# Kernel tuning notes

Measured on AMD Instinct MI355X. Metric: run time of the kernel, lower is better.

The kernel has to match this reference:

```python
import jax, jax.numpy as jnp
import numpy as np

N_NODES = 50000
N_EDGES = 25000
NNZ = 800000
IN_DIM = 256
OUT_DIM = 256


def setup_inputs() -> dict:
    key = jax.random.key(0)
    k1, k2, k3, k4, k5 = jax.random.split(key, 5)
    X = jax.random.normal(k1, (N_NODES, IN_DIM), dtype=jnp.float32)
    node_idx = jax.random.randint(k2, (NNZ,), 0, N_NODES, dtype=jnp.int64)
    edge_idx = jax.random.randint(k3, (NNZ,), 0, N_EDGES, dtype=jnp.int64)
    # Xavier-uniform-ish weight, zero bias (matches reset_parameters)
    limit = float(np.sqrt(6.0 / (IN_DIM + OUT_DIM)))
    W = jax.random.uniform(k4, (IN_DIM, OUT_DIM), dtype=jnp.float32, minval=-limit, maxval=limit)
    b = jnp.zeros((OUT_DIM,), dtype=jnp.float32)
    return {"X": X, "node_idx": node_idx, "edge_idx": edge_idx, "W": W, "b": b}


def reference(X, node_idx, edge_idx, W, b):
    # Y = X @ W + b  -- dense GEMM
    Y = X @ W + b  # [N, out_dim]

    ones = jnp.ones(node_idx.shape[0], dtype=Y.dtype)
    # D_v = rowsum(H)^-0.5 (inf -> 0); D_e = colsum(H)^-1 (inf -> 0)
    deg_v = jax.ops.segment_sum(ones, node_idx, num_segments=N_NODES)
    deg_e = jax.ops.segment_sum(ones, edge_idx, num_segments=N_EDGES)
    d_v = jnp.where(deg_v > 0, deg_v ** -0.5, 0.0)  # [N]
    d_e = jnp.where(deg_e > 0, 1.0 / deg_e, 0.0)    # [E]

    # step1 = H^T @ (D_v X): gather scaled node rows, scatter-add into edges
    Z = d_v[:, None] * Y                                   # [N, out_dim]
    step1 = jax.ops.segment_sum(Z[node_idx], edge_idx, num_segments=N_EDGES)  # [E, out_dim]
    # step2 = D_e @ step1
    step2 = d_e[:, None] * step1                           # [E, out_dim]
    # step3 = H @ step2: gather edge rows, scatter-add into nodes
    step3 = jax.ops.segment_sum(step2[edge_idx], node_idx, num_segments=N_NODES)  # [N, out_dim]
    # final = D_v @ step3
    return d_v[:, None] * step3
```

## Files before the change

### kernel.cpp

```cpp
#include <hip/hip_runtime.h>

#define N_NODES 50000
#define N_EDGES 25000
#define NNZ     800000
#define DIM     256

#define CAP_E 88
#define CAP_V 56

#define NBE 98
#define NBV 196
#define CE_COARSE 8800
#define CV_COARSE 4500
#define NNZ_PB 2048
#define P1_BLOCKS 391

#define B_A1   0
#define B_CE   0
#define B_CV   3449600
#define B_CSRE 12800000
#define B_CSRV 17200000
#define B_WT   22800000
#define B_CURV 22931072
#define B_CURE 23131072
#define B_S1B  23231072
#define B_CCUR 23331072
#define B_DV   23332248

typedef __attribute__((ext_vector_type(8))) short s8v;
typedef __attribute__((ext_vector_type(4))) float f4v;

__device__ __forceinline__ unsigned short f2bf(float f) {
    unsigned u = __float_as_uint(f);
    u = (u + 0x7FFFu + ((u >> 16) & 1u)) >> 16;
    return (unsigned short)u;
}
__device__ __forceinline__ float bf2f(unsigned short h) {
    return __uint_as_float(((unsigned)h) << 16);
}

__global__ __launch_bounds__(256) void k_prep(
        const float* __restrict__ X, const float* __restrict__ W,
        const int* __restrict__ node_idx, const int* __restrict__ edge_idx,
        unsigned short* __restrict__ Xb, unsigned short* __restrict__ WTb,
        unsigned* __restrict__ ccurE, unsigned* __restrict__ ccurV,
        unsigned* __restrict__ coarseE, unsigned* __restrict__ coarseV) {
    if (blockIdx.x < 6250) {
        size_t i = ((size_t)blockIdx.x * 256 + threadIdx.x) * 8;
        float4 p0 = *(const float4*)(X + i);
        float4 p1 = *(const float4*)(X + i + 4);
        unsigned short o[8] = {f2bf(p0.x), f2bf(p0.y), f2bf(p0.z), f2bf(p0.w),
                               f2bf(p1.x), f2bf(p1.y), f2bf(p1.z), f2bf(p1.w)};
        *(s8v*)(Xb + i) = *(const s8v*)o;
        return;
    }
    if (blockIdx.x < 6282) {
        int t = (blockIdx.x - 6250) * 256 + threadIdx.x;
        int n = t >> 5;
        int k0 = (t & 31) * 8;
        unsigned short o[8];
#pragma unroll
        for (int j = 0; j < 8; ++j) o[j] = f2bf(W[(size_t)(k0 + j) * DIM + n]);
        *(s8v*)(WTb + (size_t)n * DIM + k0) = *(const s8v*)o;
        return;
    }

    __shared__ unsigned histE[NBE], histV[NBV], baseE[NBE], baseV[NBV];
    const int tid = threadIdx.x;
    const int pb  = blockIdx.x - 6282;
    const int base = pb * NNZ_PB;

    if (tid < NBE) histE[tid] = 0;
    if (tid < NBV) histV[tid] = 0;
    __syncthreads();

    int idx0 = base + tid * 4;
    int idx1 = base + 1024 + tid * 4;
    bool ok0 = idx0 < NNZ, ok1 = idx1 < NNZ;
    int4 v0 = ok0 ? *(const int4*)(node_idx + idx0) : (int4){0,0,0,0};
    int4 e0 = ok0 ? *(const int4*)(edge_idx + idx0) : (int4){0,0,0,0};
    int4 v1 = ok1 ? *(const int4*)(node_idx + idx1) : (int4){0,0,0,0};
    int4 e1 = ok1 ? *(const int4*)(edge_idx + idx1) : (int4){0,0,0,0};
    int vv[8] = {v0.x, v0.y, v0.z, v0.w, v1.x, v1.y, v1.z, v1.w};
    int ee[8] = {e0.x, e0.y, e0.z, e0.w, e1.x, e1.y, e1.z, e1.w};

    unsigned short locE[8], locV[8];
#pragma unroll
    for (int j = 0; j < 8; ++j) {
        bool ok = (j < 4) ? ok0 : ok1;
        if (ok) {
            locE[j] = (unsigned short)atomicAdd(&histE[ee[j] >> 8], 1u);
            locV[j] = (unsigned short)atomicAdd(&histV[vv[j] >> 8], 1u);
        }
    }
    __syncthreads();
    if (tid < NBE) baseE[tid] = atomicAdd(&ccurE[tid], histE[tid]);
    if (tid < NBV) baseV[tid] = atomicAdd(&ccurV[tid], histV[tid]);
    __syncthreads();

#pragma unroll
    for (int j = 0; j < 8; ++j) {
        bool ok = (j < 4) ? ok0 : ok1;
        if (ok) {
            unsigned e = (unsigned)ee[j], v = (unsigned)vv[j];
            unsigned pe = baseE[e >> 8] + locE[j];
            if (pe < CE_COARSE)
                coarseE[(size_t)(e >> 8) * CE_COARSE + pe] = ((e & 255u) << 16) | v;
            unsigned pv = baseV[v >> 8] + locV[j];
            if (pv < CV_COARSE)
                coarseV[(size_t)(v >> 8) * CV_COARSE + pv] = ((v & 255u) << 16) | e;
        }
    }
}

__global__ __launch_bounds__(256) void k_fine(
        const unsigned* __restrict__ coarseE, const unsigned* __restrict__ coarseV,
        const unsigned* __restrict__ ccurE, const unsigned* __restrict__ ccurV,
        unsigned short* __restrict__ csrE, unsigned short* __restrict__ csrV,
        unsigned* __restrict__ cur_e, unsigned* __restrict__ cur_v,
        float* __restrict__ dv) {
    __shared__ unsigned cnt[256];
    __shared__ unsigned short slots[256 * CAP_E];
    const int tid = threadIdx.x;
    cnt[tid] = 0;
    __syncthreads();

    if (blockIdx.x < NBE) {
        int b = blockIdx.x;
        unsigned n = ccurE[b]; n = n < CE_COARSE ? n : CE_COARSE;
        const unsigned* src = coarseE + (size_t)b * CE_COARSE;
        for (unsigned i = tid; i < n; i += 256) {
            unsigned p = src[i];
            unsigned f = p >> 16, v = p & 0xFFFFu;
            unsigned pos = atomicAdd(&cnt[f], 1u);
            if (pos < CAP_E) slots[f * CAP_E + pos] = (unsigned short)v;
        }
        __syncthreads();
        int e = b * 256 + tid;
        if (e < N_EDGES) cur_e[e] = cnt[tid];
        int rows = N_EDGES - b * 256; rows = rows < 256 ? rows : 256;
        unsigned words = (unsigned)rows * (CAP_E / 2);
        unsigned* dst = (unsigned*)(csrE + (size_t)b * 256 * CAP_E);
        const unsigned* s = (const unsigned*)slots;
        for (unsigned i = tid; i < words; i += 256) dst[i] = s[i];
    } else {
        int b = blockIdx.x - NBE;
        unsigned n = ccurV[b]; n = n < CV_COARSE ? n : CV_COARSE;
        const unsigned* src = coarseV + (size_t)b * CV_COARSE;
        for (unsigned i = tid; i < n; i += 256) {
            unsigned p = src[i];
            unsigned f = p >> 16, e = p & 0xFFFFu;
            unsigned pos = atomicAdd(&cnt[f], 1u);
            if (pos < CAP_V) slots[f * CAP_V + pos] = (unsigned short)e;
        }
        __syncthreads();
        int v = b * 256 + tid;
        if (v < N_NODES) {
            unsigned c = cnt[tid];
            cur_v[v] = c;
            dv[v] = c ? __frsqrt_rn((float)c) : 0.0f;
        }
        int rows = N_NODES - b * 256; rows = rows < 256 ? rows : 256;
        unsigned words = (unsigned)rows * (CAP_V / 2);
        unsigned* dst = (unsigned*)(csrV + (size_t)b * 256 * CAP_V);
        const unsigned* s = (const unsigned*)slots;
        for (unsigned i = tid; i < words; i += 256) dst[i] = s[i];
    }
}

__global__ __launch_bounds__(256) void k_gather_edges(
        const unsigned short* __restrict__ Xb,
        const unsigned short* __restrict__ csrE,
        const unsigned* __restrict__ cur_e,
        const float* __restrict__ dv,
        unsigned short* __restrict__ A1, float* __restrict__ s1b) {
    int w = (blockIdx.x * 256 + threadIdx.x) >> 6;
    int lane = threadIdx.x & 63;
    if (w >= N_EDGES) return;
    unsigned cnt = cur_e[w]; cnt = cnt < CAP_E ? cnt : CAP_E;
    const unsigned short* lst = csrE + (size_t)w * CAP_E;
    unsigned idp = (lane < CAP_E / 2) ? ((const unsigned*)lst)[lane] : 0u;
    const unsigned short* xb = Xb + (size_t)lane * 4;

    float ax = 0.f, ay = 0.f, az = 0.f, aw = 0.f, ss = 0.f;

#define EFETCH(J, X0, X1, X2, X3, S0, S1, S2, S3)                          \
    {                                                                      \
        unsigned p0 = __shfl(idp, (int)((J) >> 1));                        \
        unsigned p1 = __shfl(idp, (int)((J) >> 1) + 1);                    \
        unsigned v0 = p0 & 0xFFFFu, v1 = p0 >> 16;                         \
        unsigned v2 = p1 & 0xFFFFu, v3 = p1 >> 16;                         \
        S0 = dv[v0]; S1 = dv[v1]; S2 = dv[v2]; S3 = dv[v3];                \
        X0 = *(const ushort4*)(xb + ((size_t)v0 << 8));                    \
        X1 = *(const ushort4*)(xb + ((size_t)v1 << 8));                    \
        X2 = *(const ushort4*)(xb + ((size_t)v2 << 8));                    \
        X3 = *(const ushort4*)(xb + ((size_t)v3 << 8));                    \
    }
#define ECONS(X0, X1, X2, X3, S0, S1, S2, S3)                              \
    {                                                                      \
        ax = fmaf(S0, bf2f(X0.x), ax); ay = fmaf(S0, bf2f(X0.y), ay);      \
        az = fmaf(S0, bf2f(X0.z), az); aw = fmaf(S0, bf2f(X0.w), aw);      \
        ax = fmaf(S1, bf2f(X1.x), ax); ay = fmaf(S1, bf2f(X1.y), ay);      \
        az = fmaf(S1, bf2f(X1.z), az); aw = fmaf(S1, bf2f(X1.w), aw);      \
        ax = fmaf(S2, bf2f(X2.x), ax); ay = fmaf(S2, bf2f(X2.y), ay);      \
        az = fmaf(S2, bf2f(X2.z), az); aw = fmaf(S2, bf2f(X2.w), aw);      \
        ax = fmaf(S3, bf2f(X3.x), ax); ay = fmaf(S3, bf2f(X3.y), ay);      \
        az = fmaf(S3, bf2f(X3.z), az); aw = fmaf(S3, bf2f(X3.w), aw);      \
        ss += (S0 + S1) + (S2 + S3);                                       \
    }

    unsigned quads = cnt >> 2;
    unsigned j = 0;
    if (quads) {
        ushort4 a0, a1, a2, a3, b0, b1, b2, b3;
        float r0, r1, r2, r3, t0, t1, t2, t3;
        EFETCH(0u, a0, a1, a2, a3, r0, r1, r2, r3);
        unsigned q = 1;
        for (; q + 1 < quads; q += 2) {
            EFETCH(4u * q,      b0, b1, b2, b3, t0, t1, t2, t3);
            ECONS(a0, a1, a2, a3, r0, r1, r2, r3);
            EFETCH(4u * q + 4u, a0, a1, a2, a3, r0, r1, r2, r3);
            ECONS(b0, b1, b2, b3, t0, t1, t2, t3);
        }
        if (q < quads) {
            EFETCH(4u * q, b0, b1, b2, b3, t0, t1, t2, t3);
            ECONS(a0, a1, a2, a3, r0, r1, r2, r3);
            ECONS(b0, b1, b2, b3, t0, t1, t2, t3);
        } else {
            ECONS(a0, a1, a2, a3, r0, r1, r2, r3);
        }
        j = quads << 2;
    }
    for (; j < cnt; ++j) {
        unsigned p = __shfl(idp, (int)(j >> 1));
        unsigned v = (j & 1) ? (p >> 16) : (p & 0xFFFFu);
        float s = dv[v];
        ushort4 x = *(const ushort4*)(xb + ((size_t)v << 8));
        ax = fmaf(s, bf2f(x.x), ax); ay = fmaf(s, bf2f(x.y), ay);
        az = fmaf(s, bf2f(x.z), az); aw = fmaf(s, bf2f(x.w), aw);
        ss += s;
    }
#undef EFETCH
#undef ECONS

    ushort4 o = {f2bf(ax), f2bf(ay), f2bf(az), f2bf(aw)};
    *(ushort4*)(A1 + (size_t)w * DIM + lane * 4) = o;
    if (lane == 0) s1b[w] = ss;
}

__global__ __launch_bounds__(256) void k_gemm_mfma(
        const unsigned short* __restrict__ A,
        const unsigned short* __restrict__ WT,
        const float* __restrict__ bias,
        const unsigned* __restrict__ cur_e,
        const float* __restrict__ s1b,
        unsigned short* __restrict__ S2) {
    const int tid  = threadIdx.x;
    const int wv   = tid >> 6;
    const int lane = tid & 63;
    const int quad = lane >> 4;
    const int l16  = lane & 15;
    const int r0   = blockIdx.x * 64;
    const int nb   = wv * 64;

    f4v acc[4][4];
#pragma unroll
    for (int mt = 0; mt < 4; ++mt)
#pragma unroll
        for (int nt = 0; nt < 4; ++nt) acc[mt][nt] = (f4v){0.f, 0.f, 0.f, 0.f};

    for (int k0 = 0; k0 < DIM; k0 += 32) {
        s8v a[4], b[4];
#pragma unroll
        for (int nt = 0; nt < 4; ++nt) {
            int n = nb + nt * 16 + l16;
            b[nt] = *(const s8v*)(WT + (size_t)n * DIM + k0 + quad * 8);
        }
#pragma unroll
        for (int mt = 0; mt < 4; ++mt) {
            int m = r0 + mt * 16 + l16;
            m = (m < N_EDGES) ? m : (N_EDGES - 1);
            a[mt] = *(const s8v*)(A + (size_t)m * DIM + k0 + quad * 8);
        }
#pragma unroll
        for (int mt = 0; mt < 4; ++mt)
#pragma unroll
            for (int nt = 0; nt < 4; ++nt)
                acc[mt][nt] = __builtin_amdgcn_mfma_f32_16x16x32_bf16(
                    a[mt], b[nt], acc[mt][nt], 0, 0, 0);
    }

    __syncthreads();

    float bv[4];
#pragma unroll
    for (int nt = 0; nt < 4; ++nt) bv[nt] = bias[nb + nt * 16 + l16];

#pragma unroll
    for (int mt = 0; mt < 4; ++mt) {
#pragma unroll
        for (int reg = 0; reg < 4; ++reg) {
            int row = r0 + mt * 16 + quad * 4 + reg;
            if (row < N_EDGES) {
                unsigned ce = cur_e[row];
                float sc = ce ? 1.0f / (float)ce : 0.0f;
                float sb = s1b[row];
#pragma unroll
                for (int nt = 0; nt < 4; ++nt) {
                    float v = sc * (acc[mt][nt][reg] + sb * bv[nt]);
                    S2[(size_t)row * DIM + nb + nt * 16 + l16] = f2bf(v);
                }
            }
        }
    }
}

__global__ __launch_bounds__(256) void k_gather_nodes(
        const unsigned short* __restrict__ S2,
        const unsigned short* __restrict__ csrV,
        const unsigned* __restrict__ cur_v,
        const float* __restrict__ dv,
        float* __restrict__ out) {
    int w = (blockIdx.x * 256 + threadIdx.x) >> 6;
    int lane = threadIdx.x & 63;
    if (w >= N_NODES) return;
    unsigned cnt = cur_v[w]; cnt = cnt < CAP_V ? cnt : CAP_V;
    const unsigned short* lst = csrV + (size_t)w * CAP_V;
    unsigned idp = (lane < CAP_V / 2) ? ((const unsigned*)lst)[lane] : 0u;
    const unsigned short* sb = S2 + (size_t)lane * 4;

    float ax = 0.f, ay = 0.f, az = 0.f, aw = 0.f;

#define NFETCH(J, X0, X1, X2, X3)                                          \
    {                                                                      \
        unsigned p0 = __shfl(idp, (int)((J) >> 1));                        \
        unsigned p1 = __shfl(idp, (int)((J) >> 1) + 1);                    \
        unsigned e0 = p0 & 0xFFFFu, e1 = p0 >> 16;                         \
        unsigned e2 = p1 & 0xFFFFu, e3 = p1 >> 16;                         \
        X0 = *(const ushort4*)(sb + ((size_t)e0 << 8));                    \
        X1 = *(const ushort4*)(sb + ((size_t)e1 << 8));                    \
        X2 = *(const ushort4*)(sb + ((size_t)e2 << 8));                    \
        X3 = *(const ushort4*)(sb + ((size_t)e3 << 8));                    \
    }
#define NCONS(X0, X1, X2, X3)                                              \
    {                                                                      \
        ax += (bf2f(X0.x) + bf2f(X1.x)) + (bf2f(X2.x) + bf2f(X3.x));       \
        ay += (bf2f(X0.y) + bf2f(X1.y)) + (bf2f(X2.y) + bf2f(X3.y));       \
        az += (bf2f(X0.z) + bf2f(X1.z)) + (bf2f(X2.z) + bf2f(X3.z));       \
        aw += (bf2f(X0.w) + bf2f(X1.w)) + (bf2f(X2.w) + bf2f(X3.w));       \
    }

    unsigned quads = cnt >> 2;
    unsigned j = 0;
    if (quads) {
        ushort4 a0, a1, a2, a3, b0, b1, b2, b3;
        NFETCH(0u, a0, a1, a2, a3);
        unsigned q = 1;
        for (; q + 1 < quads; q += 2) {
            NFETCH(4u * q,      b0, b1, b2, b3);
            NCONS(a0, a1, a2, a3);
            NFETCH(4u * q + 4u, a0, a1, a2, a3);
            NCONS(b0, b1, b2, b3);
        }
        if (q < quads) {
            NFETCH(4u * q, b0, b1, b2, b3);
            NCONS(a0, a1, a2, a3);
            NCONS(b0, b1, b2, b3);
        } else {
            NCONS(a0, a1, a2, a3);
        }
        j = quads << 2;
    }
    for (; j < cnt; ++j) {
        unsigned p = __shfl(idp, (int)(j >> 1));
        unsigned e = (j & 1) ? (p >> 16) : (p & 0xFFFFu);
        ushort4 x = *(const ushort4*)(sb + ((size_t)e << 8));
        ax += bf2f(x.x); ay += bf2f(x.y); az += bf2f(x.z); aw += bf2f(x.w);
    }
#undef NFETCH
#undef NCONS

    float s = dv[w];
    float4 o = {s * ax, s * ay, s * az, s * aw};
    *(float4*)(out + (size_t)w * DIM + lane * 4) = o;
}

extern "C" void kernel_launch(void* const* d_in, const int* in_sizes, int n_in,
                              void* d_out, int out_size, void* d_ws, size_t ws_size,
                              hipStream_t stream) {
    (void)in_sizes; (void)n_in; (void)out_size; (void)ws_size;
    const float* X        = (const float*)d_in[0];
    const int*   node_idx = (const int*)d_in[1];
    const int*   edge_idx = (const int*)d_in[2];
    const float* W        = (const float*)d_in[3];
    const float* bias     = (const float*)d_in[4];
    float* out = (float*)d_out;
    char*  ws  = (char*)d_ws;

    unsigned short* A1      = (unsigned short*)(ws + B_A1);
    unsigned*       coarseE = (unsigned*)(ws + B_CE);
    unsigned*       coarseV = (unsigned*)(ws + B_CV);
    unsigned short* csrE    = (unsigned short*)(ws + B_CSRE);
    unsigned short* csrV    = (unsigned short*)(ws + B_CSRV);
    unsigned short* WTb     = (unsigned short*)(ws + B_WT);
    unsigned*       cur_v   = (unsigned*)(ws + B_CURV);
    unsigned*       cur_e   = (unsigned*)(ws + B_CURE);
    float*          s1b     = (float*)(ws + B_S1B);
    unsigned*       ccurE   = (unsigned*)(ws + B_CCUR);
    unsigned*       ccurV   = ccurE + NBE;
    float*          dv      = (float*)(ws + B_DV);

    unsigned short* Xb = (unsigned short*)d_out;

    hipMemsetAsync(ccurE, 0, (NBE + NBV) * sizeof(unsigned), stream);

    k_prep<<<6282 + P1_BLOCKS, 256, 0, stream>>>(X, W, node_idx, edge_idx,
                                                 Xb, WTb, ccurE, ccurV, coarseE, coarseV);
    k_fine<<<NBE + NBV, 256, 0, stream>>>(coarseE, coarseV, ccurE, ccurV,
                                          csrE, csrV, cur_e, cur_v, dv);
    k_gather_edges<<<(N_EDGES * 64 + 255) / 256, 256, 0, stream>>>(
        Xb, csrE, cur_e, dv, A1, s1b);
    k_gemm_mfma<<<(N_EDGES + 63) / 64, 256, 0, stream>>>(A1, WTb, bias, cur_e, s1b, A1);
    k_gather_nodes<<<(N_NODES * 64 + 255) / 256, 256, 0, stream>>>(
        A1, csrV, cur_v, dv, out);
}
```

Before: 266.5 us.

## Stage coarse bucket scatter in shared memory and widen fine-sort blocks

In the coarse binning pass, each block now sorts its entries by bucket in shared memory using a local prefix sum, then writes them out in bucket-contiguous order. This makes the global writes more coalesced than the earlier scattered per-element stores. The fine pass is relaunched with 1024 threads per block so each block has more parallelism for its atomics and copies. The cost is about 32KB of extra shared memory in k_prep, which is also used by the conversion blocks and may lower occupancy, plus serial single-thread prefix loops.

```diff
diff --git a/kernel.cpp b/kernel.cpp
--- a/kernel.cpp
+++ b/kernel.cpp
@@ -66,6 +66,10 @@
     }
 
     __shared__ unsigned histE[NBE], histV[NBV], baseE[NBE], baseV[NBV];
+    __shared__ unsigned offE[NBE], offV[NBV];
+    __shared__ unsigned nEs, nVs;
+    __shared__ unsigned bufE[NNZ_PB], dstE[NNZ_PB];
+    __shared__ unsigned bufV[NNZ_PB], dstV[NNZ_PB];
     const int tid = threadIdx.x;
     const int pb  = blockIdx.x - 6282;
     const int base = pb * NNZ_PB;
@@ -96,6 +100,8 @@
     __syncthreads();
     if (tid < NBE) baseE[tid] = atomicAdd(&ccurE[tid], histE[tid]);
     if (tid < NBV) baseV[tid] = atomicAdd(&ccurV[tid], histV[tid]);
+    if (tid == 0) { unsigned r = 0; for (int b = 0; b < NBE; ++b) { offE[b] = r; r += histE[b]; } nEs = r; }
+    if (tid == 1) { unsigned r = 0; for (int b = 0; b < NBV; ++b) { offV[b] = r; r += histV[b]; } nVs = r; }
     __syncthreads();
 
 #pragma unroll
@@ -103,17 +109,31 @@
         bool ok = (j < 4) ? ok0 : ok1;
         if (ok) {
             unsigned e = (unsigned)ee[j], v = (unsigned)vv[j];
-            unsigned pe = baseE[e >> 8] + locE[j];
-            if (pe < CE_COARSE)
-                coarseE[(size_t)(e >> 8) * CE_COARSE + pe] = ((e & 255u) << 16) | v;
-            unsigned pv = baseV[v >> 8] + locV[j];
-            if (pv < CV_COARSE)
-                coarseV[(size_t)(v >> 8) * CV_COARSE + pv] = ((v & 255u) << 16) | e;
-        }
-    }
-}
-
-__global__ __launch_bounds__(256) void k_fine(
+            unsigned be = e >> 8, bv = v >> 8;
+            unsigned se = offE[be] + locE[j];
+            unsigned pe = baseE[be] + locE[j];
+            bufE[se] = ((e & 255u) << 16) | v;
+            dstE[se] = (pe < CE_COARSE) ? (be * CE_COARSE + pe) : 0xFFFFFFFFu;
+            unsigned sv = offV[bv] + locV[j];
+            unsigned pv = baseV[bv] + locV[j];
+            bufV[sv] = ((v & 255u) << 16) | e;
+            dstV[sv] = (pv < CV_COARSE) ? (bv * CV_COARSE + pv) : 0xFFFFFFFFu;
+        }
+    }
+    __syncthreads();
+
+    unsigned nE = nEs, nV = nVs;
+    for (unsigned i = tid; i < nE; i += 256) {
+        unsigned d = dstE[i];
+        if (d != 0xFFFFFFFFu) coarseE[d] = bufE[i];
+    }
+    for (unsigned i = tid; i < nV; i += 256) {
+        unsigned d = dstV[i];
+        if (d != 0xFFFFFFFFu) coarseV[d] = bufV[i];
+    }
+}
+
+__global__ __launch_bounds__(1024) void k_fine(
         const unsigned* __restrict__ coarseE, const unsigned* __restrict__ coarseV,
         const unsigned* __restrict__ ccurE, const unsigned* __restrict__ ccurV,
         unsigned short* __restrict__ csrE, unsigned short* __restrict__ csrV,
@@ -122,49 +142,53 @@
     __shared__ unsigned cnt[256];
     __shared__ unsigned short slots[256 * CAP_E];
     const int tid = threadIdx.x;
-    cnt[tid] = 0;
+    if (tid < 256) cnt[tid] = 0;
     __syncthreads();
 
     if (blockIdx.x < NBE) {
         int b = blockIdx.x;
         unsigned n = ccurE[b]; n = n < CE_COARSE ? n : CE_COARSE;
         const unsigned* src = coarseE + (size_t)b * CE_COARSE;
-        for (unsigned i = tid; i < n; i += 256) {
+        for (unsigned i = tid; i < n; i += 1024) {
             unsigned p = src[i];
             unsigned f = p >> 16, v = p & 0xFFFFu;
             unsigned pos = atomicAdd(&cnt[f], 1u);
             if (pos < CAP_E) slots[f * CAP_E + pos] = (unsigned short)v;
         }
         __syncthreads();
-        int e = b * 256 + tid;
-        if (e < N_EDGES) cur_e[e] = cnt[tid];
+        if (tid < 256) {
+            int e = b * 256 + tid;
+            if (e < N_EDGES) cur_e[e] = cnt[tid];
+        }
         int rows = N_EDGES - b * 256; rows = rows < 256 ? rows : 256;
         unsigned words = (unsigned)rows * (CAP_E / 2);
         unsigned* dst = (unsigned*)(csrE + (size_t)b * 256 * CAP_E);
         const unsigned* s = (const unsigned*)slots;
-        for (unsigned i = tid; i < words; i += 256) dst[i] = s[i];
+        for (unsigned i = tid; i < words; i += 1024) dst[i] = s[i];
     } else {
         int b = blockIdx.x - NBE;
         unsigned n = ccurV[b]; n = n < CV_COARSE ? n : CV_COARSE;
         const unsigned* src = coarseV + (size_t)b * CV_COARSE;
-        for (unsigned i = tid; i < n; i += 256) {
+        for (unsigned i = tid; i < n; i += 1024) {
             unsigned p = src[i];
             unsigned f = p >> 16, e = p & 0xFFFFu;
             unsigned pos = atomicAdd(&cnt[f], 1u);
             if (pos < CAP_V) slots[f * CAP_V + pos] = (unsigned short)e;
         }
         __syncthreads();
-        int v = b * 256 + tid;
-        if (v < N_NODES) {
-            unsigned c = cnt[tid];
-            cur_v[v] = c;
-            dv[v] = c ? __frsqrt_rn((float)c) : 0.0f;
+        if (tid < 256) {
+            int v = b * 256 + tid;
+            if (v < N_NODES) {
+                unsigned c = cnt[tid];
+                cur_v[v] = c;
+                dv[v] = c ? __frsqrt_rn((float)c) : 0.0f;
+            }
         }
         int rows = N_NODES - b * 256; rows = rows < 256 ? rows : 256;
         unsigned words = (unsigned)rows * (CAP_V / 2);
         unsigned* dst = (unsigned*)(csrV + (size_t)b * 256 * CAP_V);
         const unsigned* s = (const unsigned*)slots;
-        for (unsigned i = tid; i < words; i += 256) dst[i] = s[i];
+        for (unsigned i = tid; i < words; i += 1024) dst[i] = s[i];
     }
 }
 
@@ -412,12 +436,12 @@
 
     unsigned short* Xb = (unsigned short*)d_out;
 
-    hipMemsetAsync(ccurE, 0, (NBE + NBV) * sizeof(unsigned), stream);
+    (void)hipMemsetAsync(ccurE, 0, (NBE + NBV) * sizeof(unsigned), stream);
 
     k_prep<<<6282 + P1_BLOCKS, 256, 0, stream>>>(X, W, node_idx, edge_idx,
                                                  Xb, WTb, ccurE, ccurV, coarseE, coarseV);
-    k_fine<<<NBE + NBV, 256, 0, stream>>>(coarseE, coarseV, ccurE, ccurV,
-                                          csrE, csrV, cur_e, cur_v, dv);
+    k_fine<<<NBE + NBV, 1024, 0, stream>>>(coarseE, coarseV, ccurE, ccurV,
+                                           csrE, csrV, cur_e, cur_v, dv);
     k_gather_edges<<<(N_EDGES * 64 + 255) / 256, 256, 0, stream>>>(
         Xb, csrE, cur_e, dv, A1, s1b);
     k_gemm_mfma<<<(N_EDGES + 63) / 64, 256, 0, stream>>>(A1, WTb, bias, cur_e, s1b, A1);
```

Result: faster. 256.5 us, median of 2 (-3.8%).
